# Performance work log

Measured on AMD Instinct MI355X. Metric: run time of the kernel, lower is better.

Reference implementation:

```python
import jax, jax.numpy as jnp
import numpy as np

B, S, QD, KD = 8, 8192, 1024, 1024
AD = min(QD, KD)
EPS = 1e-5


def _ste(x, xq):
    # straight-through estimator: forward uses xq, gradient flows as identity
    return x + jax.lax.stop_gradient(xq - x)


def bitlinear(x, w, b):
    """BitNet b1.58-style BitLinear: ternary per-tensor weight quant,
    per-token int8 absmax activation quant, both with STE."""
    s = jnp.mean(jnp.abs(w)) + EPS                      # per-tensor weight scale
    wq = _ste(w, jnp.clip(jnp.round(w / s), -1.0, 1.0) * s)
    g = jnp.max(jnp.abs(x), axis=-1, keepdims=True) + EPS  # per-token act scale
    xq = _ste(x, jnp.clip(jnp.round(x * (127.0 / g)), -128.0, 127.0) * (g / 127.0))
    return jnp.matmul(xq, wq.T) + b


def setup_inputs() -> dict:
    key = jax.random.key(0)
    ks = jax.random.split(key, 6)
    sc = 0.02
    return {
        "query": jax.random.normal(ks[0], (B, QD), dtype=jnp.float32),
        "context_memory": jax.random.normal(ks[1], (B, S, KD), dtype=jnp.float32),
        "w_q": jax.random.normal(ks[2], (AD, QD), dtype=jnp.float32) * sc,
        "b_q": jnp.zeros((AD,), dtype=jnp.float32),
        "w_k": jax.random.normal(ks[3], (AD, KD), dtype=jnp.float32) * sc,
        "b_k": jnp.zeros((AD,), dtype=jnp.float32),
        "w_v": jax.random.normal(ks[4], (QD, KD), dtype=jnp.float32) * sc,
        "b_v": jnp.zeros((QD,), dtype=jnp.float32),
        "w_c": jax.random.normal(ks[5], (QD, 2 * QD), dtype=jnp.float32) * sc,
        "b_c": jnp.zeros((QD,), dtype=jnp.float32),
    }


def reference(query, context_memory, w_q, b_q, w_k, b_k, w_v, b_v, w_c, b_c):
    attention_dim = w_q.shape[0]
    q = bitlinear(query, w_q, b_q)                 # [B, A]
    k = bitlinear(context_memory, w_k, b_k)        # [B, S, A]
    v = bitlinear(context_memory, w_v, b_v)        # [B, S, QD]
    scores = jnp.einsum('ba,bsa->bs', q, k) / (attention_dim ** 0.5)
    attn = jax.nn.softmax(scores, axis=-1)         # [B, S]
    ctx = jnp.einsum('bs,bsq->bq', attn, v)        # [B, QD]
    combined = jnp.concatenate([query, ctx], axis=-1)  # [B, 2*QD]
    return bitlinear(combined, w_c, b_c)           # [B, QD]
```

## Files before the change

### kernel.cpp

```cpp
#include <hip/hip_runtime.h>
#include <hip/hip_bf16.h>
#include <math.h>

#define EPS 1e-5f

static constexpr int Bb = 8;
static constexpr int Ss = 8192;
static constexpr int Dd = 1024;


__device__ __forceinline__ float blk_reduce(float v, bool ismax, volatile float* lds) {
#pragma unroll
  for (int msk = 32; msk; msk >>= 1) {
    float o = __shfl_xor(v, msk);
    v = ismax ? fmaxf(v, o) : (v + o);
  }
  int w = threadIdx.x >> 6;
  __syncthreads();
  if ((threadIdx.x & 63) == 0) lds[w] = v;
  __syncthreads();
  return ismax ? fmaxf(fmaxf(lds[0], lds[1]), fmaxf(lds[2], lds[3]))
               : (lds[0] + lds[1] + lds[2] + lds[3]);
}

__device__ __forceinline__ float wred_max(float v) {
#pragma unroll
  for (int msk = 32; msk; msk >>= 1) v = fmaxf(v, __shfl_xor(v, msk));
  return v;
}

__device__ __forceinline__ float wred_sum(float v) {
#pragma unroll
  for (int msk = 32; msk; msk >>= 1) v += __shfl_xor(v, msk);
  return v;
}

__device__ __forceinline__ float quantf(float x, float c) {
  return fminf(fmaxf(rintf(x * c), -128.f), 127.f);
}

__device__ __forceinline__ float ternf(float w, float s) {
  return fminf(fmaxf(rintf(w / s), -1.f), 1.f);
}


__global__ __launch_bounds__(256) void k_abs_partial(
    const float* __restrict__ w0, const float* __restrict__ w1,
    const float* __restrict__ w2, const float* __restrict__ w3,
    double* __restrict__ part)
{
  int seg = blockIdx.x >> 6;
  int blk = blockIdx.x & 63;
  const float* w = seg == 0 ? w0 : seg == 1 ? w1 : seg == 2 ? w2 : w3;
  int n4 = (seg == 3 ? (1024 * 2048) : (1024 * 1024)) >> 2;
  const float4* w4 = (const float4*)w;
  double acc = 0.0;
  for (int i = blk * 256 + threadIdx.x; i < n4; i += 64 * 256) {
    float4 v = w4[i];
    acc += (double)fabsf(v.x) + (double)fabsf(v.y)
         + (double)fabsf(v.z) + (double)fabsf(v.w);
  }
  __shared__ double sred[256];
  sred[threadIdx.x] = acc;
  __syncthreads();
  for (int s = 128; s > 0; s >>= 1) {
    if (threadIdx.x < s) sred[threadIdx.x] += sred[threadIdx.x + s];
    __syncthreads();
  }
  if (threadIdx.x == 0) part[blockIdx.x] = sred[0];
}

__global__ void k_abs_final(const double* __restrict__ part, float* __restrict__ scales)
{
  int seg = threadIdx.x;
  if (seg >= 4) return;
  double s = 0.0;
  for (int i = 0; i < 64; i++) s += part[seg * 64 + i];
  double n = (seg == 3) ? 2097152.0 : 1048576.0;
  scales[seg] = (float)(s / n) + EPS;
}


__global__ __launch_bounds__(256) void k_quant_query(
    const float* __restrict__ x, char* __restrict__ qout, float* __restrict__ gout)
{
  __shared__ float red[4];
  int b = blockIdx.x, tid = threadIdx.x;
  float4 v = ((const float4*)(x + (size_t)b * Dd))[tid];
  float am = fmaxf(fmaxf(fabsf(v.x), fabsf(v.y)), fmaxf(fabsf(v.z), fabsf(v.w)));
  am = blk_reduce(am, true, red);
  float g = am + EPS;
  float c = 127.0f / g;
  char4 q;
  q.x = (signed char)(int)quantf(v.x, c);
  q.y = (signed char)(int)quantf(v.y, c);
  q.z = (signed char)(int)quantf(v.z, c);
  q.w = (signed char)(int)quantf(v.w, c);
  ((char4*)qout)[b * 256 + tid] = q;
  if (tid == 0) gout[b] = g;
}


__global__ __launch_bounds__(256) void k_tern_gemv_i8(
    const char* __restrict__ qact, const float* __restrict__ gact,
    const float* __restrict__ W, const float* __restrict__ bias,
    const float* __restrict__ scales, int sidx,
    float* __restrict__ out, int K, int N)
{
  int wave = blockIdx.x * 4 + (threadIdx.x >> 6);
  int lane = threadIdx.x & 63;
  int b = wave / N, o = wave - b * N;
  float s = scales[sidx];
  const float4* wr = (const float4*)(W + (size_t)o * K);
  const char4*  qr = (const char4*)(qact + (size_t)b * K);
  int n4 = K >> 2;
  float acc = 0.f;
  for (int i = lane; i < n4; i += 64) {
    float4 w4 = wr[i];
    char4  q4 = qr[i];
    acc += (float)q4.x * ternf(w4.x, s);
    acc += (float)q4.y * ternf(w4.y, s);
    acc += (float)q4.z * ternf(w4.z, s);
    acc += (float)q4.w * ternf(w4.w, s);
  }
#pragma unroll
  for (int m = 32; m; m >>= 1) acc += __shfl_xor(acc, m);
  if (lane == 0) {
    float g = gact[b];
    out[(size_t)b * N + o] = s * (g / 127.0f) * acc + bias[o];
  }
}


__global__ __launch_bounds__(256) void k_tern_gemv_f32(
    const float* __restrict__ act, const float* __restrict__ W,
    const float* __restrict__ bias, const float* __restrict__ scales, int sidx,
    float* __restrict__ out, int K, int N)
{
  int wave = blockIdx.x * 4 + (threadIdx.x >> 6);
  int lane = threadIdx.x & 63;
  int b = wave / N, o = wave - b * N;
  float s = scales[sidx];
  const float4* wr = (const float4*)(W + (size_t)o * K);
  const float4* ar = (const float4*)(act + (size_t)b * K);
  int n4 = K >> 2;
  float acc = 0.f;
  for (int i = lane; i < n4; i += 64) {
    float4 w4 = wr[i];
    float4 a4 = ar[i];
    acc += a4.x * ternf(w4.x, s);
    acc += a4.y * ternf(w4.y, s);
    acc += a4.z * ternf(w4.z, s);
    acc += a4.w * ternf(w4.w, s);
  }
#pragma unroll
  for (int m = 32; m; m >>= 1) acc += __shfl_xor(acc, m);
  if (lane == 0) out[(size_t)b * N + o] = s * acc + bias[o];
}


__global__ __launch_bounds__(256) void k_qk_part(
    const float* __restrict__ q, const float* __restrict__ Wk,
    const float* __restrict__ scales, float* __restrict__ part, int RC)
{
  __shared__ float qs[1024];
  int ch = blockIdx.x;
  int a0 = ch * RC;
  int tid = threadIdx.x;
  for (int i = tid; i < 8 * RC; i += 256) {
    int b = i / RC, a = i - b * RC;
    qs[i] = q[(size_t)b * Dd + a0 + a];
  }
  __syncthreads();
  float s = scales[1];
  float4 acc[8];
#pragma unroll
  for (int b = 0; b < 8; b++) acc[b] = make_float4(0.f, 0.f, 0.f, 0.f);
  const float4* Wr = (const float4*)(Wk + (size_t)a0 * Dd);
  for (int i = 0; i < RC; i++) {
    float4 w = Wr[(size_t)i * 256 + tid];
    float4 t;
    t.x = ternf(w.x, s); t.y = ternf(w.y, s);
    t.z = ternf(w.z, s); t.w = ternf(w.w, s);
#pragma unroll
    for (int b = 0; b < 8; b++) {
      float qb = qs[b * RC + i];
      acc[b].x += qb * t.x; acc[b].y += qb * t.y;
      acc[b].z += qb * t.z; acc[b].w += qb * t.w;
    }
  }
#pragma unroll
  for (int b = 0; b < 8; b++)
    ((float4*)part)[((size_t)ch * 8 + b) * 256 + tid] = acc[b];
}


__global__ __launch_bounds__(256) void k_qk_comb(
    const float* __restrict__ part, const float* __restrict__ q,
    const float* __restrict__ bk, const float* __restrict__ scales,
    float* __restrict__ qk, float* __restrict__ qdotbk, int NCH)
{
  __shared__ float red[4];
  int b = blockIdx.x, tid = threadIdx.x;
  float s = scales[1];
  float4 acc = make_float4(0.f, 0.f, 0.f, 0.f);
  for (int ch = 0; ch < NCH; ch++) {
    float4 p = ((const float4*)part)[((size_t)ch * 8 + b) * 256 + tid];
    acc.x += p.x; acc.y += p.y; acc.z += p.z; acc.w += p.w;
  }
  ((float4*)qk)[(size_t)b * 256 + tid] =
      make_float4(s * acc.x, s * acc.y, s * acc.z, s * acc.w);
  float p = 0.f;
  for (int a = tid; a < Dd; a += 256) p += q[(size_t)b * Dd + a] * bk[a];
  p = blk_reduce(p, false, red);
  if (tid == 0) qdotbk[b] = p;
}


__global__ __launch_bounds__(256) void k_pass(
    const float* __restrict__ X, const float* __restrict__ qk,
    const float* __restrict__ qdotbk,
    float* __restrict__ m_part, float* __restrict__ l_part,
    float* __restrict__ t_part, int NW)
{
  int b    = blockIdx.x / NW;
  int wg   = blockIdx.x - b * NW;
  int wv   = threadIdx.x >> 6;
  int lane = threadIdx.x & 63;
  int NWv  = NW * 4;
  int widx = wg * 4 + wv;
  int tok  = Ss / NWv;
  int s0   = widx * tok;

  const float4* qkb = (const float4*)(qk + (size_t)b * Dd);
  float4 qv0 = qkb[lane], qv1 = qkb[64 + lane], qv2 = qkb[128 + lane], qv3 = qkb[192 + lane];
  float qb = qdotbk[b];
  const float4* Xw = (const float4*)(X + ((size_t)b * Ss + s0) * Dd);

  float m = -INFINITY, l = 0.f;
  float4 a0 = make_float4(0,0,0,0), a1 = a0, a2 = a0, a3 = a0;

  float4 x0 = Xw[lane], x1 = Xw[64 + lane], x2 = Xw[128 + lane], x3 = Xw[192 + lane];
  for (int i = 0; i < tok; i++) {
    size_t nb = (size_t)((i + 1 < tok) ? i + 1 : i) * 256;
    float4 n0 = Xw[nb + lane], n1 = Xw[nb + 64 + lane],
           n2 = Xw[nb + 128 + lane], n3 = Xw[nb + 192 + lane];

    float am = fmaxf(
      fmaxf(fmaxf(fmaxf(fabsf(x0.x), fabsf(x0.y)), fmaxf(fabsf(x0.z), fabsf(x0.w))),
            fmaxf(fmaxf(fabsf(x1.x), fabsf(x1.y)), fmaxf(fabsf(x1.z), fabsf(x1.w)))),
      fmaxf(fmaxf(fmaxf(fabsf(x2.x), fabsf(x2.y)), fmaxf(fabsf(x2.z), fabsf(x2.w))),
            fmaxf(fmaxf(fabsf(x3.x), fabsf(x3.y)), fmaxf(fabsf(x3.z), fabsf(x3.w)))));
    am = wred_max(am);
    float g = am + EPS;
    float c = 127.0f / g;
    float gi = g / 127.0f;

    float q00 = quantf(x0.x, c), q01 = quantf(x0.y, c), q02 = quantf(x0.z, c), q03 = quantf(x0.w, c);
    float q10 = quantf(x1.x, c), q11 = quantf(x1.y, c), q12 = quantf(x1.z, c), q13 = quantf(x1.w, c);
    float q20 = quantf(x2.x, c), q21 = quantf(x2.y, c), q22 = quantf(x2.z, c), q23 = quantf(x2.w, c);
    float q30 = quantf(x3.x, c), q31 = quantf(x3.y, c), q32 = quantf(x3.z, c), q33 = quantf(x3.w, c);

    float dt = q00 * qv0.x + q01 * qv0.y + q02 * qv0.z + q03 * qv0.w
             + q10 * qv1.x + q11 * qv1.y + q12 * qv1.z + q13 * qv1.w
             + q20 * qv2.x + q21 * qv2.y + q22 * qv2.z + q23 * qv2.w
             + q30 * qv3.x + q31 * qv3.y + q32 * qv3.z + q33 * qv3.w;
    dt = wred_sum(dt);

    float score = (dt * gi + qb) * 0.03125f;
    float mn  = fmaxf(m, score);
    float scl = expf(m - mn);
    float p   = expf(score - mn);
    l = l * scl + p;
    float cf = p * gi;
    a0.x = a0.x * scl + cf * q00; a0.y = a0.y * scl + cf * q01;
    a0.z = a0.z * scl + cf * q02; a0.w = a0.w * scl + cf * q03;
    a1.x = a1.x * scl + cf * q10; a1.y = a1.y * scl + cf * q11;
    a1.z = a1.z * scl + cf * q12; a1.w = a1.w * scl + cf * q13;
    a2.x = a2.x * scl + cf * q20; a2.y = a2.y * scl + cf * q21;
    a2.z = a2.z * scl + cf * q22; a2.w = a2.w * scl + cf * q23;
    a3.x = a3.x * scl + cf * q30; a3.y = a3.y * scl + cf * q31;
    a3.z = a3.z * scl + cf * q32; a3.w = a3.w * scl + cf * q33;
    m = mn;
    x0 = n0; x1 = n1; x2 = n2; x3 = n3;
  }

  size_t pidx = (size_t)b * NWv + widx;
  float4* tpw = (float4*)t_part + (size_t)pidx * 256;
  tpw[lane] = a0; tpw[64 + lane] = a1; tpw[128 + lane] = a2; tpw[192 + lane] = a3;
  if (lane == 0) { m_part[pidx] = m; l_part[pidx] = l; }
}


__global__ __launch_bounds__(256) void k_ml(
    const float* __restrict__ m_part, const float* __restrict__ l_part,
    float* __restrict__ ML, int NWv)
{
  __shared__ float red[4];
  int b = blockIdx.x, tid = threadIdx.x;
  float mi = -INFINITY;
  for (int i = tid; i < NWv; i += 256) mi = fmaxf(mi, m_part[(size_t)b * NWv + i]);
  float M = blk_reduce(mi, true, red);
  float li = 0.f;
  for (int i = tid; i < NWv; i += 256)
    li += l_part[(size_t)b * NWv + i] * expf(m_part[(size_t)b * NWv + i] - M);
  float L = blk_reduce(li, false, red);
  if (tid == 0) { ML[b * 2] = M; ML[b * 2 + 1] = L; }
}


__global__ __launch_bounds__(256) void k_combA(
    const float* __restrict__ m_part, const float* __restrict__ t_part,
    const float* __restrict__ ML, float* __restrict__ t16, int NWv)
{
  int b = blockIdx.x >> 4, k = blockIdx.x & 15;
  int grp = NWv >> 4;
  int tid = threadIdx.x;
  float M = ML[b * 2];
  float4 acc = make_float4(0,0,0,0);
  for (int i = 0; i < grp; i++) {
    size_t pi = (size_t)b * NWv + k * grp + i;
    float w = expf(m_part[pi] - M);
    float4 tp = ((const float4*)t_part)[pi * 256 + tid];
    acc.x += w * tp.x; acc.y += w * tp.y; acc.z += w * tp.z; acc.w += w * tp.w;
  }
  ((float4*)t16)[((size_t)(b * 16 + k)) * 256 + tid] = acc;
}


__global__ __launch_bounds__(256) void k_combB(
    const float* __restrict__ t16, const float* __restrict__ ML,
    float* __restrict__ t)
{
  int b = blockIdx.x, tid = threadIdx.x;
  float invL = 1.0f / ML[b * 2 + 1];
  float4 acc = make_float4(0,0,0,0);
  for (int k = 0; k < 16; k++) {
    float4 v = ((const float4*)t16)[((size_t)(b * 16 + k)) * 256 + tid];
    acc.x += v.x; acc.y += v.y; acc.z += v.z; acc.w += v.w;
  }
  ((float4*)t)[(size_t)b * 256 + tid] =
      make_float4(acc.x * invL, acc.y * invL, acc.z * invL, acc.w * invL);
}


__global__ __launch_bounds__(256) void k_quant_comb(
    const float* __restrict__ query, const float* __restrict__ ctx,
    char* __restrict__ qout, float* __restrict__ gout)
{
  __shared__ float red[4];
  int b = blockIdx.x, tid = threadIdx.x;
  float4 vq = ((const float4*)(query + (size_t)b * Dd))[tid];
  float4 vc = ((const float4*)(ctx   + (size_t)b * Dd))[tid];
  float am = fmaxf(
      fmaxf(fmaxf(fabsf(vq.x), fabsf(vq.y)), fmaxf(fabsf(vq.z), fabsf(vq.w))),
      fmaxf(fmaxf(fabsf(vc.x), fabsf(vc.y)), fmaxf(fabsf(vc.z), fabsf(vc.w))));
  am = blk_reduce(am, true, red);
  float g = am + EPS;
  float c = 127.0f / g;
  char4 a, d;
  a.x = (signed char)(int)quantf(vq.x, c);
  a.y = (signed char)(int)quantf(vq.y, c);
  a.z = (signed char)(int)quantf(vq.z, c);
  a.w = (signed char)(int)quantf(vq.w, c);
  d.x = (signed char)(int)quantf(vc.x, c);
  d.y = (signed char)(int)quantf(vc.y, c);
  d.z = (signed char)(int)quantf(vc.z, c);
  d.w = (signed char)(int)quantf(vc.w, c);
  ((char4*)qout)[b * 512 + tid] = a;
  ((char4*)qout)[b * 512 + 256 + tid] = d;
  if (tid == 0) gout[b] = g;
}


extern "C" void kernel_launch(void* const* d_in, const int* in_sizes, int n_in,
                              void* d_out, int out_size, void* d_ws, size_t ws_size,
                              hipStream_t stream)
{
  const float* query = (const float*)d_in[0];
  const float* X     = (const float*)d_in[1];
  const float* w_q   = (const float*)d_in[2];
  const float* b_q   = (const float*)d_in[3];
  const float* w_k   = (const float*)d_in[4];
  const float* b_k   = (const float*)d_in[5];
  const float* w_v   = (const float*)d_in[6];
  const float* b_v   = (const float*)d_in[7];
  const float* w_c   = (const float*)d_in[8];
  const float* b_c   = (const float*)d_in[9];
  float* out = (float*)d_out;
  char* ws = (char*)d_ws;

  size_t off = 0;
  auto alloc = [&](size_t bytes) -> size_t {
    size_t o = off;
    off += (bytes + 255) & ~(size_t)255;
    return o;
  };
  auto align256 = [](size_t bytes) -> size_t {
    return (bytes + 255) & ~(size_t)255;
  };
  size_t o_part   = alloc(256 * sizeof(double));
  size_t o_scales = alloc(4 * sizeof(float));
  size_t o_gq     = alloc(Bb * sizeof(float));
  size_t o_qq     = alloc((size_t)Bb * Dd);
  size_t o_q      = alloc((size_t)Bb * Dd * 4);
  size_t o_qk     = alloc((size_t)Bb * Dd * 4);
  size_t o_qbk    = alloc(Bb * sizeof(float));
  size_t o_t      = alloc((size_t)Bb * Dd * 4);
  size_t o_ctx    = alloc((size_t)Bb * Dd * 4);
  size_t o_gc     = alloc(Bb * sizeof(float));
  size_t o_qc     = alloc((size_t)Bb * 2 * Dd);
  size_t o_ML     = alloc(Bb * 2 * sizeof(float));
  size_t o_t16    = alloc((size_t)Bb * 16 * Dd * 4);
  size_t base_end = off;

  int NCH = 64;
  for (;;) {
    size_t need = base_end
      + align256((size_t)NCH * 8 * Dd * 4)
      + align256((size_t)Bb * 64 * 4) * 2
      + align256((size_t)Bb * 64 * Dd * 4);
    if (need <= ws_size || NCH == 8) break;
    NCH >>= 1;
  }
  int RC = Dd / NCH;
  size_t o_qkp = alloc((size_t)NCH * 8 * Dd * 4);
  size_t qkp_end = off;

  int NW = 128;
  for (;;) {
    size_t NWv_ = (size_t)NW * 4;
    size_t need = qkp_end
      + align256((size_t)Bb * NWv_ * 4) * 2
      + align256((size_t)Bb * NWv_ * Dd * 4);
    if (need <= ws_size || NW == 16) break;
    NW >>= 1;
  }
  int NWv = NW * 4;
  size_t o_mp = alloc((size_t)Bb * NWv * 4);
  size_t o_lp = alloc((size_t)Bb * NWv * 4);
  size_t o_tp = alloc((size_t)Bb * NWv * Dd * 4);

  double* part   = (double*)(ws + o_part);
  float*  scales = (float*)(ws + o_scales);
  float*  gq     = (float*)(ws + o_gq);
  char*   qq     = (char*)(ws + o_qq);
  float*  qv     = (float*)(ws + o_q);
  float*  qk     = (float*)(ws + o_qk);
  float*  qbk    = (float*)(ws + o_qbk);
  float*  tvec   = (float*)(ws + o_t);
  float*  ctx    = (float*)(ws + o_ctx);
  float*  gc     = (float*)(ws + o_gc);
  char*   qc     = (char*)(ws + o_qc);
  float*  ML     = (float*)(ws + o_ML);
  float*  t16    = (float*)(ws + o_t16);
  float*  qkp    = (float*)(ws + o_qkp);
  float*  mp     = (float*)(ws + o_mp);
  float*  lp     = (float*)(ws + o_lp);
  float*  tp     = (float*)(ws + o_tp);

  k_abs_partial<<<256, 256, 0, stream>>>(w_q, w_k, w_v, w_c, part);
  k_abs_final<<<1, 64, 0, stream>>>(part, scales);
  k_quant_query<<<Bb, 256, 0, stream>>>(query, qq, gq);
  k_tern_gemv_i8<<<(Bb * Dd) / 4, 256, 0, stream>>>(qq, gq, w_q, b_q, scales, 0, qv, Dd, Dd);
  k_qk_part<<<NCH, 256, 0, stream>>>(qv, w_k, scales, qkp, RC);
  k_qk_comb<<<Bb, 256, 0, stream>>>(qkp, qv, b_k, scales, qk, qbk, NCH);
  k_pass<<<Bb * NW, 256, 0, stream>>>(X, qk, qbk, mp, lp, tp, NW);
  k_ml<<<Bb, 256, 0, stream>>>(mp, lp, ML, NWv);
  k_combA<<<Bb * 16, 256, 0, stream>>>(mp, tp, ML, t16, NWv);
  k_combB<<<Bb, 256, 0, stream>>>(t16, ML, tvec);
  k_tern_gemv_f32<<<(Bb * Dd) / 4, 256, 0, stream>>>(tvec, w_v, b_v, scales, 2, ctx, Dd, Dd);
  k_quant_comb<<<Bb, 256, 0, stream>>>(query, ctx, qc, gc);
  k_tern_gemv_i8<<<(Bb * Dd) / 4, 256, 0, stream>>>(qc, gc, w_c, b_c, scales, 3, out, 2 * Dd, Dd);
}
```

Measured before the change: 144.1 us.

## Fuse small kernels via atomic last-block reductions and fold quantization into GEMVs

Cuts the launch chain from thirteen kernels to seven. The scale finalization moves into the abs-sum kernel through a last-block atomic counter. Query and combined-vector quantization are folded into their ternary GEMVs using shared memory, and the qk partial reduction plus the softmax combine stages are merged using atomic counters, with a spin-wait grid barrier in k_qk. Workspace sizing is fixed at NW=64 and NCH=64, and the online softmax takes a branch so it needs only one exp per token. The changes aim to remove per-launch overhead and intermediate buffers, at the cost of relying on all 64 k_qk blocks being co-resident and on a memset of the counters every call.

```diff
diff --git a/kernel.cpp b/kernel.cpp
--- a/kernel.cpp
+++ b/kernel.cpp
@@ -7,6 +7,11 @@
 static constexpr int Bb = 8;
 static constexpr int Ss = 8192;
 static constexpr int Dd = 1024;
+static constexpr int NW = 64;
+static constexpr int NWv = NW * 4;
+static constexpr int TOK = Ss / NWv;
+static constexpr int NCH = 64;
+static constexpr int RC = Dd / NCH;
 
 
 __device__ __forceinline__ float blk_reduce(float v, bool ismax, volatile float* lds) {
@@ -44,10 +49,10 @@
 }
 
 
-__global__ __launch_bounds__(256) void k_abs_partial(
+__global__ __launch_bounds__(256) void k_scales(
     const float* __restrict__ w0, const float* __restrict__ w1,
     const float* __restrict__ w2, const float* __restrict__ w3,
-    double* __restrict__ part)
+    double* __restrict__ part, float* __restrict__ scales, int* __restrict__ cnt)
 {
   int seg = blockIdx.x >> 6;
   int blk = blockIdx.x & 63;
@@ -67,67 +72,244 @@
     if (threadIdx.x < s) sred[threadIdx.x] += sred[threadIdx.x + s];
     __syncthreads();
   }
-  if (threadIdx.x == 0) part[blockIdx.x] = sred[0];
-}
-
-__global__ void k_abs_final(const double* __restrict__ part, float* __restrict__ scales)
-{
-  int seg = threadIdx.x;
-  if (seg >= 4) return;
-  double s = 0.0;
-  for (int i = 0; i < 64; i++) s += part[seg * 64 + i];
-  double n = (seg == 3) ? 2097152.0 : 1048576.0;
-  scales[seg] = (float)(s / n) + EPS;
-}
-
-
-__global__ __launch_bounds__(256) void k_quant_query(
-    const float* __restrict__ x, char* __restrict__ qout, float* __restrict__ gout)
-{
+  __shared__ int lastold;
+  if (threadIdx.x == 0) {
+    part[blockIdx.x] = sred[0];
+    __threadfence();
+    lastold = atomicAdd(cnt, 1);
+  }
+  __syncthreads();
+  if (lastold == 255) {
+    __threadfence();
+    if (threadIdx.x < 4) {
+      int sg = threadIdx.x;
+      double s = 0.0;
+      for (int i = 0; i < 64; i++) s += part[sg * 64 + i];
+      double n = (sg == 3) ? 2097152.0 : 1048576.0;
+      scales[sg] = (float)(s / n) + EPS;
+    }
+  }
+}
+
+
+__global__ __launch_bounds__(256) void k_qgemv(
+    const float* __restrict__ query, const float* __restrict__ W,
+    const float* __restrict__ bias, const float* __restrict__ scales,
+    float* __restrict__ out)
+{
+  __shared__ float cs[Dd];
   __shared__ float red[4];
-  int b = blockIdx.x, tid = threadIdx.x;
-  float4 v = ((const float4*)(x + (size_t)b * Dd))[tid];
+  int b = blockIdx.x >> 8, grp = blockIdx.x & 255;
+  int tid = threadIdx.x, wv = tid >> 6, lane = tid & 63;
+  float4 v = ((const float4*)(query + (size_t)b * Dd))[tid];
   float am = fmaxf(fmaxf(fabsf(v.x), fabsf(v.y)), fmaxf(fabsf(v.z), fabsf(v.w)));
   am = blk_reduce(am, true, red);
   float g = am + EPS;
   float c = 127.0f / g;
-  char4 q;
-  q.x = (signed char)(int)quantf(v.x, c);
-  q.y = (signed char)(int)quantf(v.y, c);
-  q.z = (signed char)(int)quantf(v.z, c);
-  q.w = (signed char)(int)quantf(v.w, c);
-  ((char4*)qout)[b * 256 + tid] = q;
-  if (tid == 0) gout[b] = g;
-}
-
-
-__global__ __launch_bounds__(256) void k_tern_gemv_i8(
-    const char* __restrict__ qact, const float* __restrict__ gact,
-    const float* __restrict__ W, const float* __restrict__ bias,
-    const float* __restrict__ scales, int sidx,
-    float* __restrict__ out, int K, int N)
-{
-  int wave = blockIdx.x * 4 + (threadIdx.x >> 6);
+  float4 qv = make_float4(quantf(v.x, c), quantf(v.y, c), quantf(v.z, c), quantf(v.w, c));
+  ((float4*)cs)[tid] = qv;
+  __syncthreads();
+  float s = scales[0];
+  int o = grp * 4 + wv;
+  const float4* wr = (const float4*)(W + (size_t)o * Dd);
+  float acc = 0.f;
+#pragma unroll
+  for (int i = 0; i < 4; i++) {
+    int idx = i * 64 + lane;
+    float4 w4 = wr[idx];
+    float4 a4 = ((const float4*)cs)[idx];
+    acc += a4.x * ternf(w4.x, s) + a4.y * ternf(w4.y, s)
+         + a4.z * ternf(w4.z, s) + a4.w * ternf(w4.w, s);
+  }
+  acc = wred_sum(acc);
+  if (lane == 0) out[(size_t)b * Dd + o] = s * (g / 127.0f) * acc + bias[o];
+}
+
+
+__global__ __launch_bounds__(256) void k_qk(
+    const float* __restrict__ q, const float* __restrict__ Wk,
+    const float* __restrict__ bk, const float* __restrict__ scales,
+    float* __restrict__ part, float* __restrict__ qk, float* __restrict__ qdotbk,
+    int* __restrict__ cnt)
+{
+  __shared__ float qs[Bb * RC];
+  int ch = blockIdx.x;
+  int a0 = ch * RC;
+  int tid = threadIdx.x;
+  if (tid < Bb * RC) {
+    int b = tid / RC, a = tid - b * RC;
+    qs[tid] = q[(size_t)b * Dd + a0 + a];
+  }
+  __syncthreads();
+  float s = scales[1];
+  float4 acc[Bb];
+#pragma unroll
+  for (int b = 0; b < Bb; b++) acc[b] = make_float4(0.f, 0.f, 0.f, 0.f);
+  const float4* Wr = (const float4*)(Wk + (size_t)a0 * Dd);
+  for (int i = 0; i < RC; i++) {
+    float4 w = Wr[(size_t)i * 256 + tid];
+    float4 t;
+    t.x = ternf(w.x, s); t.y = ternf(w.y, s);
+    t.z = ternf(w.z, s); t.w = ternf(w.w, s);
+#pragma unroll
+    for (int b = 0; b < Bb; b++) {
+      float qb = qs[b * RC + i];
+      acc[b].x += qb * t.x; acc[b].y += qb * t.y;
+      acc[b].z += qb * t.z; acc[b].w += qb * t.w;
+    }
+  }
+#pragma unroll
+  for (int b = 0; b < Bb; b++)
+    ((float4*)part)[((size_t)ch * Bb + b) * 256 + tid] = acc[b];
+
+  __threadfence();
+  if (tid == 0) {
+    atomicAdd(cnt, 1);
+    while (__hip_atomic_load(cnt, __ATOMIC_ACQUIRE, __HIP_MEMORY_SCOPE_AGENT) < NCH) {
+      __builtin_amdgcn_s_sleep(8);
+    }
+  }
+  __syncthreads();
+  __threadfence();
+
+  int b = blockIdx.x >> 3, dc = blockIdx.x & 7;
+  if (tid < 32) {
+    int d4 = dc * 32 + tid;
+    float4 a = make_float4(0.f, 0.f, 0.f, 0.f);
+    for (int k = 0; k < NCH; k++) {
+      float4 p = ((const float4*)part)[((size_t)k * Bb + b) * 256 + d4];
+      a.x += p.x; a.y += p.y; a.z += p.z; a.w += p.w;
+    }
+    ((float4*)qk)[(size_t)b * 256 + d4] = make_float4(s * a.x, s * a.y, s * a.z, s * a.w);
+  } else if (dc == 0 && tid >= 64 && tid < 128) {
+    int lane = tid - 64;
+    float p = 0.f;
+    for (int a = lane; a < Dd; a += 64) p += q[(size_t)b * Dd + a] * bk[a];
+    p = wred_sum(p);
+    if (lane == 0) qdotbk[b] = p;
+  }
+}
+
+
+__global__ __launch_bounds__(256) void k_pass(
+    const float* __restrict__ X, const float* __restrict__ qk,
+    const float* __restrict__ qdotbk,
+    float* __restrict__ m_part, float* __restrict__ l_part,
+    float* __restrict__ t_part)
+{
+  int b    = blockIdx.x >> 6;
+  int wg   = blockIdx.x & 63;
+  int wv   = threadIdx.x >> 6;
   int lane = threadIdx.x & 63;
-  int b = wave / N, o = wave - b * N;
-  float s = scales[sidx];
-  const float4* wr = (const float4*)(W + (size_t)o * K);
-  const char4*  qr = (const char4*)(qact + (size_t)b * K);
-  int n4 = K >> 2;
-  float acc = 0.f;
-  for (int i = lane; i < n4; i += 64) {
-    float4 w4 = wr[i];
-    char4  q4 = qr[i];
-    acc += (float)q4.x * ternf(w4.x, s);
-    acc += (float)q4.y * ternf(w4.y, s);
-    acc += (float)q4.z * ternf(w4.z, s);
-    acc += (float)q4.w * ternf(w4.w, s);
-  }
-#pragma unroll
-  for (int m = 32; m; m >>= 1) acc += __shfl_xor(acc, m);
-  if (lane == 0) {
-    float g = gact[b];
-    out[(size_t)b * N + o] = s * (g / 127.0f) * acc + bias[o];
+  int widx = wg * 4 + wv;
+  int s0   = widx * TOK;
+
+  const float4* qkb = (const float4*)(qk + (size_t)b * Dd);
+  float4 qv0 = qkb[lane], qv1 = qkb[64 + lane], qv2 = qkb[128 + lane], qv3 = qkb[192 + lane];
+  float qb = qdotbk[b];
+  const float4* Xw = (const float4*)(X + ((size_t)b * Ss + s0) * Dd);
+
+  float m = -INFINITY, l = 0.f;
+  float4 a0 = make_float4(0,0,0,0), a1 = a0, a2 = a0, a3 = a0;
+
+  float4 x0 = Xw[lane], x1 = Xw[64 + lane], x2 = Xw[128 + lane], x3 = Xw[192 + lane];
+  for (int i = 0; i < TOK; i++) {
+    size_t nb = (size_t)((i + 1 < TOK) ? i + 1 : i) * 256;
+    float4 n0 = Xw[nb + lane], n1 = Xw[nb + 64 + lane],
+           n2 = Xw[nb + 128 + lane], n3 = Xw[nb + 192 + lane];
+
+    float am = fmaxf(
+      fmaxf(fmaxf(fmaxf(fabsf(x0.x), fabsf(x0.y)), fmaxf(fabsf(x0.z), fabsf(x0.w))),
+            fmaxf(fmaxf(fabsf(x1.x), fabsf(x1.y)), fmaxf(fabsf(x1.z), fabsf(x1.w)))),
+      fmaxf(fmaxf(fmaxf(fabsf(x2.x), fabsf(x2.y)), fmaxf(fabsf(x2.z), fabsf(x2.w))),
+            fmaxf(fmaxf(fabsf(x3.x), fabsf(x3.y)), fmaxf(fabsf(x3.z), fabsf(x3.w)))));
+    am = wred_max(am);
+    float g = am + EPS;
+    float c = 127.0f / g;
+    float gi = g / 127.0f;
+
+    float q00 = quantf(x0.x, c), q01 = quantf(x0.y, c), q02 = quantf(x0.z, c), q03 = quantf(x0.w, c);
+    float q10 = quantf(x1.x, c), q11 = quantf(x1.y, c), q12 = quantf(x1.z, c), q13 = quantf(x1.w, c);
+    float q20 = quantf(x2.x, c), q21 = quantf(x2.y, c), q22 = quantf(x2.z, c), q23 = quantf(x2.w, c);
+    float q30 = quantf(x3.x, c), q31 = quantf(x3.y, c), q32 = quantf(x3.z, c), q33 = quantf(x3.w, c);
+
+    float dt = q00 * qv0.x + q01 * qv0.y + q02 * qv0.z + q03 * qv0.w
+             + q10 * qv1.x + q11 * qv1.y + q12 * qv1.z + q13 * qv1.w
+             + q20 * qv2.x + q21 * qv2.y + q22 * qv2.z + q23 * qv2.w
+             + q30 * qv3.x + q31 * qv3.y + q32 * qv3.z + q33 * qv3.w;
+    dt = wred_sum(dt);
+
+    float score = (dt * gi + qb) * 0.03125f;
+    if (score <= m) {
+      float p  = expf(score - m);
+      l += p;
+      float cf = p * gi;
+      a0.x += cf * q00; a0.y += cf * q01; a0.z += cf * q02; a0.w += cf * q03;
+      a1.x += cf * q10; a1.y += cf * q11; a1.z += cf * q12; a1.w += cf * q13;
+      a2.x += cf * q20; a2.y += cf * q21; a2.z += cf * q22; a2.w += cf * q23;
+      a3.x += cf * q30; a3.y += cf * q31; a3.z += cf * q32; a3.w += cf * q33;
+    } else {
+      float scl = expf(m - score);
+      l = l * scl + 1.0f;
+      float cf = gi;
+      a0.x = a0.x * scl + cf * q00; a0.y = a0.y * scl + cf * q01;
+      a0.z = a0.z * scl + cf * q02; a0.w = a0.w * scl + cf * q03;
+      a1.x = a1.x * scl + cf * q10; a1.y = a1.y * scl + cf * q11;
+      a1.z = a1.z * scl + cf * q12; a1.w = a1.w * scl + cf * q13;
+      a2.x = a2.x * scl + cf * q20; a2.y = a2.y * scl + cf * q21;
+      a2.z = a2.z * scl + cf * q22; a2.w = a2.w * scl + cf * q23;
+      a3.x = a3.x * scl + cf * q30; a3.y = a3.y * scl + cf * q31;
+      a3.z = a3.z * scl + cf * q32; a3.w = a3.w * scl + cf * q33;
+      m = score;
+    }
+    x0 = n0; x1 = n1; x2 = n2; x3 = n3;
+  }
+
+  size_t pidx = (size_t)b * NWv + widx;
+  float4* tpw = (float4*)t_part + (size_t)pidx * 256;
+  tpw[lane] = a0; tpw[64 + lane] = a1; tpw[128 + lane] = a2; tpw[192 + lane] = a3;
+  if (threadIdx.x == (unsigned)(wv << 6)) { m_part[pidx] = m; l_part[pidx] = l; }
+}
+
+
+__global__ __launch_bounds__(256) void k_comb(
+    const float* __restrict__ m_part, const float* __restrict__ l_part,
+    const float* __restrict__ t_part, float* __restrict__ t16,
+    float* __restrict__ t, int* __restrict__ cnt)
+{
+  __shared__ float red[4];
+  int b = blockIdx.x >> 4, k = blockIdx.x & 15;
+  int tid = threadIdx.x;
+  float mi = m_part[(size_t)b * NWv + tid];
+  float M = blk_reduce(mi, true, red);
+  float li = l_part[(size_t)b * NWv + tid] * expf(mi - M);
+  float L = blk_reduce(li, false, red);
+
+  float4 acc = make_float4(0,0,0,0);
+  for (int i = 0; i < 16; i++) {
+    size_t pi = (size_t)b * NWv + k * 16 + i;
+    float w = expf(m_part[pi] - M);
+    float4 tp = ((const float4*)t_part)[pi * 256 + tid];
+    acc.x += w * tp.x; acc.y += w * tp.y; acc.z += w * tp.z; acc.w += w * tp.w;
+  }
+  ((float4*)t16)[((size_t)(b * 16 + k)) * 256 + tid] = acc;
+
+  __shared__ int lastold;
+  if (tid == 0) {
+    __threadfence();
+    lastold = atomicAdd(&cnt[b], 1);
+  }
+  __syncthreads();
+  if (lastold == 15) {
+    __threadfence();
+    float invL = 1.0f / L;
+    float4 a = make_float4(0,0,0,0);
+    for (int kk = 0; kk < 16; kk++) {
+      float4 v = ((const float4*)t16)[((size_t)(b * 16 + kk)) * 256 + tid];
+      a.x += v.x; a.y += v.y; a.z += v.z; a.w += v.w;
+    }
+    ((float4*)t)[(size_t)b * 256 + tid] =
+        make_float4(a.x * invL, a.y * invL, a.z * invL, a.w * invL);
   }
 }
 
@@ -148,208 +330,23 @@
   for (int i = lane; i < n4; i += 64) {
     float4 w4 = wr[i];
     float4 a4 = ar[i];
-    acc += a4.x * ternf(w4.x, s);
-    acc += a4.y * ternf(w4.y, s);
-    acc += a4.z * ternf(w4.z, s);
-    acc += a4.w * ternf(w4.w, s);
-  }
-#pragma unroll
-  for (int m = 32; m; m >>= 1) acc += __shfl_xor(acc, m);
+    acc += a4.x * ternf(w4.x, s) + a4.y * ternf(w4.y, s)
+         + a4.z * ternf(w4.z, s) + a4.w * ternf(w4.w, s);
+  }
+  acc = wred_sum(acc);
   if (lane == 0) out[(size_t)b * N + o] = s * acc + bias[o];
 }
 
 
-__global__ __launch_bounds__(256) void k_qk_part(
-    const float* __restrict__ q, const float* __restrict__ Wk,
-    const float* __restrict__ scales, float* __restrict__ part, int RC)
-{
-  __shared__ float qs[1024];
-  int ch = blockIdx.x;
-  int a0 = ch * RC;
-  int tid = threadIdx.x;
-  for (int i = tid; i < 8 * RC; i += 256) {
-    int b = i / RC, a = i - b * RC;
-    qs[i] = q[(size_t)b * Dd + a0 + a];
-  }
-  __syncthreads();
-  float s = scales[1];
-  float4 acc[8];
-#pragma unroll
-  for (int b = 0; b < 8; b++) acc[b] = make_float4(0.f, 0.f, 0.f, 0.f);
-  const float4* Wr = (const float4*)(Wk + (size_t)a0 * Dd);
-  for (int i = 0; i < RC; i++) {
-    float4 w = Wr[(size_t)i * 256 + tid];
-    float4 t;
-    t.x = ternf(w.x, s); t.y = ternf(w.y, s);
-    t.z = ternf(w.z, s); t.w = ternf(w.w, s);
-#pragma unroll
-    for (int b = 0; b < 8; b++) {
-      float qb = qs[b * RC + i];
-      acc[b].x += qb * t.x; acc[b].y += qb * t.y;
-      acc[b].z += qb * t.z; acc[b].w += qb * t.w;
-    }
-  }
-#pragma unroll
-  for (int b = 0; b < 8; b++)
-    ((float4*)part)[((size_t)ch * 8 + b) * 256 + tid] = acc[b];
-}
-
-
-__global__ __launch_bounds__(256) void k_qk_comb(
-    const float* __restrict__ part, const float* __restrict__ q,
-    const float* __restrict__ bk, const float* __restrict__ scales,
-    float* __restrict__ qk, float* __restrict__ qdotbk, int NCH)
-{
+__global__ __launch_bounds__(256) void k_final(
+    const float* __restrict__ query, const float* __restrict__ ctx,
+    const float* __restrict__ W, const float* __restrict__ bias,
+    const float* __restrict__ scales, float* __restrict__ out)
+{
+  __shared__ float cs[2 * Dd];
   __shared__ float red[4];
-  int b = blockIdx.x, tid = threadIdx.x;
-  float s = scales[1];
-  float4 acc = make_float4(0.f, 0.f, 0.f, 0.f);
-  for (int ch = 0; ch < NCH; ch++) {
-    float4 p = ((const float4*)part)[((size_t)ch * 8 + b) * 256 + tid];
-    acc.x += p.x; acc.y += p.y; acc.z += p.z; acc.w += p.w;
-  }
-  ((float4*)qk)[(size_t)b * 256 + tid] =
-      make_float4(s * acc.x, s * acc.y, s * acc.z, s * acc.w);
-  float p = 0.f;
-  for (int a = tid; a < Dd; a += 256) p += q[(size_t)b * Dd + a] * bk[a];
-  p = blk_reduce(p, false, red);
-  if (tid == 0) qdotbk[b] = p;
-}
-
-
-__global__ __launch_bounds__(256) void k_pass(
-    const float* __restrict__ X, const float* __restrict__ qk,
-    const float* __restrict__ qdotbk,
-    float* __restrict__ m_part, float* __restrict__ l_part,
-    float* __restrict__ t_part, int NW)
-{
-  int b    = blockIdx.x / NW;
-  int wg   = blockIdx.x - b * NW;
-  int wv   = threadIdx.x >> 6;
-  int lane = threadIdx.x & 63;
-  int NWv  = NW * 4;
-  int widx = wg * 4 + wv;
-  int tok  = Ss / NWv;
-  int s0   = widx * tok;
-
-  const float4* qkb = (const float4*)(qk + (size_t)b * Dd);
-  float4 qv0 = qkb[lane], qv1 = qkb[64 + lane], qv2 = qkb[128 + lane], qv3 = qkb[192 + lane];
-  float qb = qdotbk[b];
-  const float4* Xw = (const float4*)(X + ((size_t)b * Ss + s0) * Dd);
-
-  float m = -INFINITY, l = 0.f;
-  float4 a0 = make_float4(0,0,0,0), a1 = a0, a2 = a0, a3 = a0;
-
-  float4 x0 = Xw[lane], x1 = Xw[64 + lane], x2 = Xw[128 + lane], x3 = Xw[192 + lane];
-  for (int i = 0; i < tok; i++) {
-    size_t nb = (size_t)((i + 1 < tok) ? i + 1 : i) * 256;
-    float4 n0 = Xw[nb + lane], n1 = Xw[nb + 64 + lane],
-           n2 = Xw[nb + 128 + lane], n3 = Xw[nb + 192 + lane];
-
-    float am = fmaxf(
-      fmaxf(fmaxf(fmaxf(fabsf(x0.x), fabsf(x0.y)), fmaxf(fabsf(x0.z), fabsf(x0.w))),
-            fmaxf(fmaxf(fabsf(x1.x), fabsf(x1.y)), fmaxf(fabsf(x1.z), fabsf(x1.w)))),
-      fmaxf(fmaxf(fmaxf(fabsf(x2.x), fabsf(x2.y)), fmaxf(fabsf(x2.z), fabsf(x2.w))),
-            fmaxf(fmaxf(fabsf(x3.x), fabsf(x3.y)), fmaxf(fabsf(x3.z), fabsf(x3.w)))));
-    am = wred_max(am);
-    float g = am + EPS;
-    float c = 127.0f / g;
-    float gi = g / 127.0f;
-
-    float q00 = quantf(x0.x, c), q01 = quantf(x0.y, c), q02 = quantf(x0.z, c), q03 = quantf(x0.w, c);
-    float q10 = quantf(x1.x, c), q11 = quantf(x1.y, c), q12 = quantf(x1.z, c), q13 = quantf(x1.w, c);
-    float q20 = quantf(x2.x, c), q21 = quantf(x2.y, c), q22 = quantf(x2.z, c), q23 = quantf(x2.w, c);
-    float q30 = quantf(x3.x, c), q31 = quantf(x3.y, c), q32 = quantf(x3.z, c), q33 = quantf(x3.w, c);
-
-    float dt = q00 * qv0.x + q01 * qv0.y + q02 * qv0.z + q03 * qv0.w
-             + q10 * qv1.x + q11 * qv1.y + q12 * qv1.z + q13 * qv1.w
-             + q20 * qv2.x + q21 * qv2.y + q22 * qv2.z + q23 * qv2.w
-             + q30 * qv3.x + q31 * qv3.y + q32 * qv3.z + q33 * qv3.w;
-    dt = wred_sum(dt);
-
-    float score = (dt * gi + qb) * 0.03125f;
-    float mn  = fmaxf(m, score);
-    float scl = expf(m - mn);
-    float p   = expf(score - mn);
-    l = l * scl + p;
-    float cf = p * gi;
-    a0.x = a0.x * scl + cf * q00; a0.y = a0.y * scl + cf * q01;
-    a0.z = a0.z * scl + cf * q02; a0.w = a0.w * scl + cf * q03;
-    a1.x = a1.x * scl + cf * q10; a1.y = a1.y * scl + cf * q11;
-    a1.z = a1.z * scl + cf * q12; a1.w = a1.w * scl + cf * q13;
-    a2.x = a2.x * scl + cf * q20; a2.y = a2.y * scl + cf * q21;
-    a2.z = a2.z * scl + cf * q22; a2.w = a2.w * scl + cf * q23;
-    a3.x = a3.x * scl + cf * q30; a3.y = a3.y * scl + cf * q31;
-    a3.z = a3.z * scl + cf * q32; a3.w = a3.w * scl + cf * q33;
-    m = mn;
-    x0 = n0; x1 = n1; x2 = n2; x3 = n3;
-  }
-
-  size_t pidx = (size_t)b * NWv + widx;
-  float4* tpw = (float4*)t_part + (size_t)pidx * 256;
-  tpw[lane] = a0; tpw[64 + lane] = a1; tpw[128 + lane] = a2; tpw[192 + lane] = a3;
-  if (lane == 0) { m_part[pidx] = m; l_part[pidx] = l; }
-}
-
-
-__global__ __launch_bounds__(256) void k_ml(
-    const float* __restrict__ m_part, const float* __restrict__ l_part,
-    float* __restrict__ ML, int NWv)
-{
-  __shared__ float red[4];
-  int b = blockIdx.x, tid = threadIdx.x;
-  float mi = -INFINITY;
-  for (int i = tid; i < NWv; i += 256) mi = fmaxf(mi, m_part[(size_t)b * NWv + i]);
-  float M = blk_reduce(mi, true, red);
-  float li = 0.f;
-  for (int i = tid; i < NWv; i += 256)
-    li += l_part[(size_t)b * NWv + i] * expf(m_part[(size_t)b * NWv + i] - M);
-  float L = blk_reduce(li, false, red);
-  if (tid == 0) { ML[b * 2] = M; ML[b * 2 + 1] = L; }
-}
-
-
-__global__ __launch_bounds__(256) void k_combA(
-    const float* __restrict__ m_part, const float* __restrict__ t_part,
-    const float* __restrict__ ML, float* __restrict__ t16, int NWv)
-{
-  int b = blockIdx.x >> 4, k = blockIdx.x & 15;
-  int grp = NWv >> 4;
-  int tid = threadIdx.x;
-  float M = ML[b * 2];
-  float4 acc = make_float4(0,0,0,0);
-  for (int i = 0; i < grp; i++) {
-    size_t pi = (size_t)b * NWv + k * grp + i;
-    float w = expf(m_part[pi] - M);
-    float4 tp = ((const float4*)t_part)[pi * 256 + tid];
-    acc.x += w * tp.x; acc.y += w * tp.y; acc.z += w * tp.z; acc.w += w * tp.w;
-  }
-  ((float4*)t16)[((size_t)(b * 16 + k)) * 256 + tid] = acc;
-}
-
-
-__global__ __launch_bounds__(256) void k_combB(
-    const float* __restrict__ t16, const float* __restrict__ ML,
-    float* __restrict__ t)
-{
-  int b = blockIdx.x, tid = threadIdx.x;
-  float invL = 1.0f / ML[b * 2 + 1];
-  float4 acc = make_float4(0,0,0,0);
-  for (int k = 0; k < 16; k++) {
-    float4 v = ((const float4*)t16)[((size_t)(b * 16 + k)) * 256 + tid];
-    acc.x += v.x; acc.y += v.y; acc.z += v.z; acc.w += v.w;
-  }
-  ((float4*)t)[(size_t)b * 256 + tid] =
-      make_float4(acc.x * invL, acc.y * invL, acc.z * invL, acc.w * invL);
-}
-
-
-__global__ __launch_bounds__(256) void k_quant_comb(
-    const float* __restrict__ query, const float* __restrict__ ctx,
-    char* __restrict__ qout, float* __restrict__ gout)
-{
-  __shared__ float red[4];
-  int b = blockIdx.x, tid = threadIdx.x;
+  int b = blockIdx.x >> 8, grp = blockIdx.x & 255;
+  int tid = threadIdx.x, wv = tid >> 6, lane = tid & 63;
   float4 vq = ((const float4*)(query + (size_t)b * Dd))[tid];
   float4 vc = ((const float4*)(ctx   + (size_t)b * Dd))[tid];
   float am = fmaxf(
@@ -358,18 +355,23 @@
   am = blk_reduce(am, true, red);
   float g = am + EPS;
   float c = 127.0f / g;
-  char4 a, d;
-  a.x = (signed char)(int)quantf(vq.x, c);
-  a.y = (signed char)(int)quantf(vq.y, c);
-  a.z = (signed char)(int)quantf(vq.z, c);
-  a.w = (signed char)(int)quantf(vq.w, c);
-  d.x = (signed char)(int)quantf(vc.x, c);
-  d.y = (signed char)(int)quantf(vc.y, c);
-  d.z = (signed char)(int)quantf(vc.z, c);
-  d.w = (signed char)(int)quantf(vc.w, c);
-  ((char4*)qout)[b * 512 + tid] = a;
-  ((char4*)qout)[b * 512 + 256 + tid] = d;
-  if (tid == 0) gout[b] = g;
+  ((float4*)cs)[tid] = make_float4(quantf(vq.x, c), quantf(vq.y, c), quantf(vq.z, c), quantf(vq.w, c));
+  ((float4*)cs)[256 + tid] = make_float4(quantf(vc.x, c), quantf(vc.y, c), quantf(vc.z, c), quantf(vc.w, c));
+  __syncthreads();
+  float s = scales[3];
+  int o = grp * 4 + wv;
+  const float4* wr = (const float4*)(W + (size_t)o * 2 * Dd);
+  float acc = 0.f;
+#pragma unroll
+  for (int i = 0; i < 8; i++) {
+    int idx = i * 64 + lane;
+    float4 w4 = wr[idx];
+    float4 a4 = ((const float4*)cs)[idx];
+    acc += a4.x * ternf(w4.x, s) + a4.y * ternf(w4.y, s)
+         + a4.z * ternf(w4.z, s) + a4.w * ternf(w4.w, s);
+  }
+  acc = wred_sum(acc);
+  if (lane == 0) out[(size_t)b * Dd + o] = s * (g / 127.0f) * acc + bias[o];
 }
 
 
@@ -396,80 +398,41 @@
     off += (bytes + 255) & ~(size_t)255;
     return o;
   };
-  auto align256 = [](size_t bytes) -> size_t {
-    return (bytes + 255) & ~(size_t)255;
-  };
+  size_t o_cnt    = alloc(256);
   size_t o_part   = alloc(256 * sizeof(double));
   size_t o_scales = alloc(4 * sizeof(float));
-  size_t o_gq     = alloc(Bb * sizeof(float));
-  size_t o_qq     = alloc((size_t)Bb * Dd);
   size_t o_q      = alloc((size_t)Bb * Dd * 4);
   size_t o_qk     = alloc((size_t)Bb * Dd * 4);
   size_t o_qbk    = alloc(Bb * sizeof(float));
   size_t o_t      = alloc((size_t)Bb * Dd * 4);
   size_t o_ctx    = alloc((size_t)Bb * Dd * 4);
-  size_t o_gc     = alloc(Bb * sizeof(float));
-  size_t o_qc     = alloc((size_t)Bb * 2 * Dd);
-  size_t o_ML     = alloc(Bb * 2 * sizeof(float));
   size_t o_t16    = alloc((size_t)Bb * 16 * Dd * 4);
-  size_t base_end = off;
-
-  int NCH = 64;
-  for (;;) {
-    size_t need = base_end
-      + align256((size_t)NCH * 8 * Dd * 4)
-      + align256((size_t)Bb * 64 * 4) * 2
-      + align256((size_t)Bb * 64 * Dd * 4);
-    if (need <= ws_size || NCH == 8) break;
-    NCH >>= 1;
-  }
-  int RC = Dd / NCH;
-  size_t o_qkp = alloc((size_t)NCH * 8 * Dd * 4);
-  size_t qkp_end = off;
-
-  int NW = 128;
-  for (;;) {
-    size_t NWv_ = (size_t)NW * 4;
-    size_t need = qkp_end
-      + align256((size_t)Bb * NWv_ * 4) * 2
-      + align256((size_t)Bb * NWv_ * Dd * 4);
-    if (need <= ws_size || NW == 16) break;
-    NW >>= 1;
-  }
-  int NWv = NW * 4;
-  size_t o_mp = alloc((size_t)Bb * NWv * 4);
-  size_t o_lp = alloc((size_t)Bb * NWv * 4);
-  size_t o_tp = alloc((size_t)Bb * NWv * Dd * 4);
-
+  size_t o_qkp    = alloc((size_t)NCH * Bb * Dd * 4);
+  size_t o_mp     = alloc((size_t)Bb * NWv * 4);
+  size_t o_lp     = alloc((size_t)Bb * NWv * 4);
+  size_t o_tp     = alloc((size_t)Bb * NWv * Dd * 4);
+  (void)ws_size;
+
+  int*    cnt    = (int*)(ws + o_cnt);
   double* part   = (double*)(ws + o_part);
   float*  scales = (float*)(ws + o_scales);
-  float*  gq     = (float*)(ws + o_gq);
-  char*   qq     = (char*)(ws + o_qq);
   float*  qv     = (float*)(ws + o_q);
   float*  qk     = (float*)(ws + o_qk);
   float*  qbk    = (float*)(ws + o_qbk);
   float*  tvec   = (float*)(ws + o_t);
   float*  ctx    = (float*)(ws + o_ctx);
-  float*  gc     = (float*)(ws + o_gc);
-  char*   qc     = (char*)(ws + o_qc);
-  float*  ML     = (float*)(ws + o_ML);
   float*  t16    = (float*)(ws + o_t16);
   float*  qkp    = (float*)(ws + o_qkp);
   float*  mp     = (float*)(ws + o_mp);
   float*  lp     = (float*)(ws + o_lp);
   float*  tp     = (float*)(ws + o_tp);
 
-  k_abs_partial<<<256, 256, 0, stream>>>(w_q, w_k, w_v, w_c, part);
-  k_abs_final<<<1, 64, 0, stream>>>(part, scales);
-  k_quant_query<<<Bb, 256, 0, stream>>>(query, qq, gq);
-  k_tern_gemv_i8<<<(Bb * Dd) / 4, 256, 0, stream>>>(qq, gq, w_q, b_q, scales, 0, qv, Dd, Dd);
-  k_qk_part<<<NCH, 256, 0, stream>>>(qv, w_k, scales, qkp, RC);
-  k_qk_comb<<<Bb, 256, 0, stream>>>(qkp, qv, b_k, scales, qk, qbk, NCH);
-  k_pass<<<Bb * NW, 256, 0, stream>>>(X, qk, qbk, mp, lp, tp, NW);
-  k_ml<<<Bb, 256, 0, stream>>>(mp, lp, ML, NWv);
-  k_combA<<<Bb * 16, 256, 0, stream>>>(mp, tp, ML, t16, NWv);
-  k_combB<<<Bb, 256, 0, stream>>>(t16, ML, tvec);
+  hipMemsetAsync(ws + o_cnt, 0, 256, stream);
+  k_scales<<<256, 256, 0, stream>>>(w_q, w_k, w_v, w_c, part, scales, &cnt[0]);
+  k_qgemv<<<Bb * 256, 256, 0, stream>>>(query, w_q, b_q, scales, qv);
+  k_qk<<<NCH, 256, 0, stream>>>(qv, w_k, b_k, scales, qkp, qk, qbk, &cnt[1]);
+  k_pass<<<Bb * NW, 256, 0, stream>>>(X, qk, qbk, mp, lp, tp);
+  k_comb<<<Bb * 16, 256, 0, stream>>>(mp, lp, tp, t16, tvec, &cnt[2]);
   k_tern_gemv_f32<<<(Bb * Dd) / 4, 256, 0, stream>>>(tvec, w_v, b_v, scales, 2, ctx, Dd, Dd);
-  k_quant_comb<<<Bb, 256, 0, stream>>>(query, ctx, qc, gc);
-  k_tern_gemv_i8<<<(Bb * Dd) / 4, 256, 0, stream>>>(qc, gc, w_c, b_c, scales, 3, out, 2 * Dd, Dd);
-}
+  k_final<<<Bb * 256, 256, 0, stream>>>(query, ctx, w_c, b_c, scales, out);
+}
```

New measurement: 135.7 us. -5.8%, faster.
